# Kernel tuning notes

Hardware: AMD Instinct MI355X
Metric: run time of the kernel (lower is better)

Reference implementation:

```python
import jax, jax.numpy as jnp
import numpy as np

N, DIM = 512, 64
SIZE, QUANT = 3.0, 0.25
LXY = int((2 * SIZE + 1e-4) // QUANT)   # 24
LZ = int((2 * 2 + 1e-4) // QUANT)       # 16


def setup_inputs() -> dict:
    key = jax.random.key(0)
    ks = jax.random.split(key, 16)
    s = lambda d: 1.0 / np.sqrt(d)
    feat = jax.random.normal(ks[0], (N, DIM), jnp.float32)
    dxy = jax.random.uniform(ks[1], (N, N, 2), jnp.float32, -SIZE, SIZE)
    dz = jax.random.uniform(ks[2], (N, N, 1), jnp.float32, -2.0, 2.0)
    distance = jnp.concatenate([dxy, dz], axis=-1)
    return {
        "feat": feat,
        "distance": distance,
        "W_qkv": jax.random.normal(ks[3], (DIM, 3 * DIM), jnp.float32) * s(DIM),
        "b_qkv": jnp.zeros((3 * DIM,), jnp.float32),
        "Wg1": jax.random.normal(ks[4], (DIM, DIM), jnp.float32) * s(DIM),
        "bg1": jnp.zeros((DIM,), jnp.float32),
        "Wg2": jax.random.normal(ks[5], (DIM, DIM), jnp.float32) * s(DIM),
        "bg2": jnp.zeros((DIM,), jnp.float32),
        "table_x": jax.random.normal(ks[6], (3, LXY, DIM), jnp.float32) * 0.02,
        "table_y": jax.random.normal(ks[7], (3, LXY, DIM), jnp.float32) * 0.02,
        "table_z": jax.random.normal(ks[8], (3, LZ, DIM), jnp.float32) * 0.02,
        "Wd": jax.random.normal(ks[9], (3 * DIM, DIM), jnp.float32) * s(3 * DIM),
        "bd": jnp.zeros((DIM,), jnp.float32),
        "ln_g": jnp.ones((DIM,), jnp.float32),
        "ln_b": jnp.zeros((DIM,), jnp.float32),
    }


def _quant_idx(distance):
    ixy = jnp.minimum((distance[:, :, :2] + SIZE) // QUANT, 2.0 * SIZE / QUANT - 1)
    iz = jnp.minimum((distance[:, :, 2:] + 2.0) // QUANT, 4.0 / QUANT - 1)
    return jnp.concatenate([ixy, iz], axis=-1).astype(jnp.int32)  # [N,N,3]


def _vec_att(feat, idx, W_qkv, b_qkv, Wg1, bg1, Wg2, bg2, table_x, table_y, table_z):
    n, dim = feat.shape
    qkv = (feat @ W_qkv + b_qkv).reshape(n, 3, dim)
    q, k, v = qkv[:, 0], qkv[:, 1], qkv[:, 2]
    # relation MLP on pairwise q-k differences: [N,N,dim]
    rel = q[:, None, :] - k[None, :, :]
    rel = jnp.maximum(rel @ Wg1 + bg1, 0.0) @ Wg2 + bg2
    ix, iy, iz = idx[:, :, 0], idx[:, :, 1], idx[:, :, 2]
    enc_q = table_x[0][ix] + table_y[0][iy] + table_z[0][iz]
    enc_k = table_x[1][ix] + table_y[1][iy] + table_z[1][iz]
    enc_v = table_x[2][ix] + table_y[2][iy] + table_z[2][iz]
    rel = rel + q[:, None, :] * enc_q + k[None, :, :] * enc_k
    vv = v[None, :, :] + enc_v
    weights = jax.nn.softmax(rel, axis=1)
    return jnp.sum(weights * vv, axis=1)  # [N,dim]


def reference(feat, distance, W_qkv, b_qkv, Wg1, bg1, Wg2, bg2,
              table_x, table_y, table_z, Wd, bd, ln_g, ln_b):
    idx = _quant_idx(distance)
    att = _vec_att(feat, idx, W_qkv, b_qkv, Wg1, bg1, Wg2, bg2,
                   table_x, table_y, table_z)
    n = att.shape[0]
    mean_rep = jnp.broadcast_to(jnp.mean(att, axis=0, keepdims=True), att.shape)
    max_rep = jnp.broadcast_to(jnp.max(att, axis=0, keepdims=True), att.shape)
    x = jnp.concatenate([att, mean_rep, max_rep], axis=-1)  # [N, 3*dim]
    h = x @ Wd + bd
    mu = jnp.mean(h, axis=-1, keepdims=True)
    var = jnp.mean((h - mu) ** 2, axis=-1, keepdims=True)
    h = (h - mu) * jax.lax.rsqrt(var + 1e-5) * ln_g + ln_b
    return jnp.maximum(h, 0.0)
```

## Files before the change

kernel.cpp:

```cpp
#include <hip/hip_runtime.h>
#include <hip/hip_bf16.h>
#include <math.h>

#define N 512
#define DIM 64

typedef __attribute__((ext_vector_type(8))) short short8;
typedef __attribute__((ext_vector_type(4))) float f32x4;

#define WS_Q 0
#define WS_K (N*DIM)
#define WS_V (2*N*DIM)
#define WS_A (3*N*DIM)
#define WS_B (4*N*DIM)
#define WS_ATT (5*N*DIM)
#define WS_MEAN (6*N*DIM)
#define WS_MAXK (6*N*DIM + DIM)

__device__ __forceinline__ unsigned short f2bf(float f) {
    unsigned u = __float_as_uint(f);
    return (unsigned short)((u + 0x7fffu + ((u >> 16) & 1u)) >> 16);
}

__global__ void k_qkv(const float* __restrict__ feat, const float* __restrict__ Wqkv,
                      const float* __restrict__ bqkv, const float* __restrict__ Wg1,
                      const float* __restrict__ bg1, float* __restrict__ ws) {
    __shared__ float frow[DIM];
    __shared__ float qrow[DIM];
    __shared__ float krow[DIM];
    int i = blockIdx.x;
    int c = threadIdx.x;
    if (i == 0 && c < DIM) {
        ws[WS_MEAN + c] = 0.0f;
        ((unsigned*)ws)[WS_MAXK + c] = 0u;
    }
    if (c < DIM) frow[c] = feat[i * DIM + c];
    __syncthreads();
    float acc = bqkv[c];
#pragma unroll
    for (int kk = 0; kk < DIM; ++kk) acc += frow[kk] * Wqkv[kk * 3 * DIM + c];
    if (c < DIM) {
        ws[WS_Q + i * DIM + c] = acc;
        qrow[c] = acc;
    } else if (c < 2 * DIM) {
        ws[WS_K + i * DIM + (c - DIM)] = acc;
        krow[c - DIM] = acc;
    } else {
        ws[WS_V + i * DIM + (c - 2 * DIM)] = acc;
    }
    __syncthreads();
    if (c < DIM) {
        float a = bg1[c];
#pragma unroll
        for (int kk = 0; kk < DIM; ++kk) a += qrow[kk] * Wg1[kk * DIM + c];
        ws[WS_A + i * DIM + c] = a;
    } else if (c < 2 * DIM) {
        int cc = c - DIM;
        float b = 0.0f;
#pragma unroll
        for (int kk = 0; kk < DIM; ++kk) b += krow[kk] * Wg1[kk * DIM + cc];
        ws[WS_B + i * DIM + cc] = b;
    }
}

__global__ __launch_bounds__(256, 2) void k_attn(
    const float* __restrict__ dist,
    const float* __restrict__ tx, const float* __restrict__ ty,
    const float* __restrict__ tz, const float* __restrict__ Wg2,
    const float* __restrict__ bg2, float* __restrict__ ws) {
    __shared__ float stx[3 * 24 * 65];
    __shared__ float sty[3 * 24 * 65];
    __shared__ float stz[3 * 16 * 65];
    __shared__ int sidx[N];
    __shared__ float smrg[4][4][16][3];

    const int i = blockIdx.x;
    const int tid = threadIdx.x;
    const int w = tid >> 6;
    const int lane = tid & 63;
    const int l15 = lane & 15;
    const int kg = lane >> 4;

    for (int t = tid; t < 3 * 24 * 64; t += 256) {
        int row = t >> 6, col = t & 63;
        stx[row * 65 + col] = tx[t];
        sty[row * 65 + col] = ty[t];
    }
    for (int t = tid; t < 3 * 16 * 64; t += 256) {
        int row = t >> 6, col = t & 63;
        stz[row * 65 + col] = tz[t];
    }
    for (int j = tid; j < N; j += 256) {
        const float* dp = dist + ((size_t)i * N + j) * 3;
        int ix = min((int)floorf((dp[0] + 3.0f) * 4.0f), 23);
        int iy = min((int)floorf((dp[1] + 3.0f) * 4.0f), 23);
        int iz = min((int)floorf((dp[2] + 2.0f) * 4.0f), 15);
        sidx[j] = ix | (iy << 5) | (iz << 10);
    }

    short8 wB[2][4];
#pragma unroll
    for (int ks = 0; ks < 2; ++ks)
#pragma unroll
        for (int n = 0; n < 4; ++n) {
            union { short8 v; unsigned short u[8]; } tmp;
#pragma unroll
            for (int e = 0; e < 8; ++e)
                tmp.u[e] = f2bf(Wg2[(ks * 32 + kg * 8 + e) * DIM + n * 16 + l15]);
            wB[ks][n] = tmp.v;
        }

    float af[16];
    {
        const float* ap = ws + WS_A + i * DIM + kg * 8;
#pragma unroll
        for (int e = 0; e < 8; ++e) { af[e] = ap[e]; af[8 + e] = ap[32 + e]; }
    }
    float qr[4], br[4];
#pragma unroll
    for (int n = 0; n < 4; ++n) {
        qr[n] = ws[WS_Q + i * DIM + n * 16 + l15];
        br[n] = bg2[n * 16 + l15];
    }

    const float* Bp = ws + WS_B;
    const float* Kp = ws + WS_K;
    const float* Vp = ws + WS_V;

    float stm[4], stl[4], sta[4];
#pragma unroll
    for (int n = 0; n < 4; ++n) { stm[n] = -INFINITY; stl[n] = 0.f; sta[n] = 0.f; }

    __syncthreads();

    const float LOG2E = 1.4426950408889634f;

    for (int cb = 0; cb < N; cb += 64) {
        int jA = cb + w * 16 + l15;
        const float* bb = Bp + jA * DIM + kg * 8;
        union { short8 v; unsigned short u[8]; } h0, h1;
#pragma unroll
        for (int e = 0; e < 8; ++e) {
            h0.u[e] = f2bf(fmaxf(af[e] - bb[e], 0.f));
            h1.u[e] = f2bf(fmaxf(af[8 + e] - bb[32 + e], 0.f));
        }
        f32x4 acc[4];
#pragma unroll
        for (int n = 0; n < 4; ++n) {
            acc[n] = (f32x4)(0.f);
            acc[n] = __builtin_amdgcn_mfma_f32_16x16x32_bf16(h0.v, wB[0][n], acc[n], 0, 0, 0);
            acc[n] = __builtin_amdgcn_mfma_f32_16x16x32_bf16(h1.v, wB[1][n], acc[n], 0, 0, 0);
        }
        int j0 = cb + w * 16 + kg * 4;
        int pk[4];
#pragma unroll
        for (int r = 0; r < 4; ++r) pk[r] = sidx[j0 + r];
#pragma unroll
        for (int n = 0; n < 4; ++n) {
            int dof = n * 16 + l15;
            float rel2[4], vvv[4];
#pragma unroll
            for (int r = 0; r < 4; ++r) {
                int ix = pk[r] & 31, iy = (pk[r] >> 5) & 31, iz = pk[r] >> 10;
                float eq = stx[ix * 65 + dof] + sty[iy * 65 + dof] + stz[iz * 65 + dof];
                float ek = stx[(24 + ix) * 65 + dof] + sty[(24 + iy) * 65 + dof] +
                           stz[(16 + iz) * 65 + dof];
                float ev = stx[(48 + ix) * 65 + dof] + sty[(48 + iy) * 65 + dof] +
                           stz[(32 + iz) * 65 + dof];
                int j = j0 + r;
                float kv = Kp[j * DIM + dof];
                float vv = Vp[j * DIM + dof];
                float rel = acc[n][r] + br[n] + qr[n] * eq + kv * ek;
                rel2[r] = rel * LOG2E;
                vvv[r] = vv + ev;
            }
            float mx = fmaxf(fmaxf(rel2[0], rel2[1]), fmaxf(rel2[2], rel2[3]));
            float mn = fmaxf(stm[n], mx);
            float sc = exp2f(stm[n] - mn);
            float sl = 0.f, sa = 0.f;
#pragma unroll
            for (int r = 0; r < 4; ++r) {
                float p = exp2f(rel2[r] - mn);
                sl += p;
                sa += p * vvv[r];
            }
            stl[n] = stl[n] * sc + sl;
            sta[n] = sta[n] * sc + sa;
            stm[n] = mn;
        }
    }

#pragma unroll
    for (int n = 0; n < 4; ++n) {
#pragma unroll
        for (int off = 16; off <= 32; off <<= 1) {
            float om = __shfl_xor(stm[n], off);
            float ol = __shfl_xor(stl[n], off);
            float oa = __shfl_xor(sta[n], off);
            float mn = fmaxf(stm[n], om);
            float s1 = exp2f(stm[n] - mn), s2 = exp2f(om - mn);
            stl[n] = stl[n] * s1 + ol * s2;
            sta[n] = sta[n] * s1 + oa * s2;
            stm[n] = mn;
        }
        if (lane < 16) {
            smrg[w][n][l15][0] = stm[n];
            smrg[w][n][l15][1] = stl[n];
            smrg[w][n][l15][2] = sta[n];
        }
    }
    __syncthreads();
    if (tid < DIM) {
        int n = tid >> 4, c = tid & 15;
        float m = smrg[0][n][c][0], l = smrg[0][n][c][1], a = smrg[0][n][c][2];
#pragma unroll
        for (int ww = 1; ww < 4; ++ww) {
            float om = smrg[ww][n][c][0], ol = smrg[ww][n][c][1], oa = smrg[ww][n][c][2];
            float mn = fmaxf(m, om);
            float s1 = exp2f(m - mn), s2 = exp2f(om - mn);
            l = l * s1 + ol * s2;
            a = a * s1 + oa * s2;
            m = mn;
        }
        float att = a / l;
        ws[WS_ATT + i * DIM + tid] = att;
        atomicAdd(ws + WS_MEAN + tid, att);
        unsigned u = __float_as_uint(att);
        unsigned key = (u & 0x80000000u) ? ~u : (u | 0x80000000u);
        atomicMax((unsigned*)ws + WS_MAXK + tid, key);
    }
}

__global__ void k_final(const float* __restrict__ ws, const float* __restrict__ Wd,
                        const float* __restrict__ bd, const float* __restrict__ lng,
                        const float* __restrict__ lnb, float* __restrict__ out) {
    __shared__ float xs[3 * DIM];
    int i = blockIdx.x;
    int c = threadIdx.x;
    xs[c] = ws[WS_ATT + i * DIM + c];
    xs[DIM + c] = ws[WS_MEAN + c] * (1.0f / (float)N);
    unsigned key = ((const unsigned*)ws)[WS_MAXK + c];
    unsigned ub = (key & 0x80000000u) ? (key & 0x7fffffffu) : ~key;
    xs[2 * DIM + c] = __uint_as_float(ub);
    __syncthreads();
    float h = bd[c];
#pragma unroll
    for (int kk = 0; kk < 3 * DIM; ++kk) h += xs[kk] * Wd[kk * DIM + c];
    float s = h;
#pragma unroll
    for (int off = 32; off >= 1; off >>= 1) s += __shfl_xor(s, off);
    float mu = s * (1.0f / DIM);
    float dif = h - mu;
    float s2 = dif * dif;
#pragma unroll
    for (int off = 32; off >= 1; off >>= 1) s2 += __shfl_xor(s2, off);
    float var = s2 * (1.0f / DIM);
    float rs = rsqrtf(var + 1e-5f);
    float o = dif * rs * lng[c] + lnb[c];
    out[i * DIM + c] = fmaxf(o, 0.0f);
}

extern "C" void kernel_launch(void* const* d_in, const int* in_sizes, int n_in,
                              void* d_out, int out_size, void* d_ws, size_t ws_size,
                              hipStream_t stream) {
    (void)in_sizes; (void)n_in; (void)out_size; (void)ws_size;
    const float* feat = (const float*)d_in[0];
    const float* dist = (const float*)d_in[1];
    const float* Wqkv = (const float*)d_in[2];
    const float* bqkv = (const float*)d_in[3];
    const float* Wg1  = (const float*)d_in[4];
    const float* bg1  = (const float*)d_in[5];
    const float* Wg2  = (const float*)d_in[6];
    const float* bg2  = (const float*)d_in[7];
    const float* tx   = (const float*)d_in[8];
    const float* ty   = (const float*)d_in[9];
    const float* tz   = (const float*)d_in[10];
    const float* Wd   = (const float*)d_in[11];
    const float* bd   = (const float*)d_in[12];
    const float* lng  = (const float*)d_in[13];
    const float* lnb  = (const float*)d_in[14];
    float* ws = (float*)d_ws;
    float* out = (float*)d_out;

    hipLaunchKernelGGL(k_qkv, dim3(N), dim3(192), 0, stream, feat, Wqkv, bqkv, Wg1, bg1, ws);
    hipLaunchKernelGGL(k_attn, dim3(N), dim3(256), 0, stream, dist, tx, ty, tz, Wg2, bg2, ws);
    hipLaunchKernelGGL(k_final, dim3(N), dim3(64), 0, stream, ws, Wd, bd, lng, lnb, out);
}
```

Measured before the change: 141.5 us.

## Pack q/k tables as bf16 pairs, fold log2e, widen attention and final blocks

```diff
diff --git a/kernel.cpp b/kernel.cpp
--- a/kernel.cpp
+++ b/kernel.cpp
@@ -36,9 +36,15 @@
     }
     if (c < DIM) frow[c] = feat[i * DIM + c];
     __syncthreads();
-    float acc = bqkv[c];
-#pragma unroll
-    for (int kk = 0; kk < DIM; ++kk) acc += frow[kk] * Wqkv[kk * 3 * DIM + c];
+    float a0 = bqkv[c], a1 = 0.f, a2 = 0.f, a3 = 0.f;
+#pragma unroll
+    for (int kk = 0; kk < DIM; kk += 4) {
+        a0 += frow[kk + 0] * Wqkv[(kk + 0) * 3 * DIM + c];
+        a1 += frow[kk + 1] * Wqkv[(kk + 1) * 3 * DIM + c];
+        a2 += frow[kk + 2] * Wqkv[(kk + 2) * 3 * DIM + c];
+        a3 += frow[kk + 3] * Wqkv[(kk + 3) * 3 * DIM + c];
+    }
+    float acc = (a0 + a1) + (a2 + a3);
     if (c < DIM) {
         ws[WS_Q + i * DIM + c] = acc;
         qrow[c] = acc;
@@ -49,30 +55,36 @@
         ws[WS_V + i * DIM + (c - 2 * DIM)] = acc;
     }
     __syncthreads();
-    if (c < DIM) {
-        float a = bg1[c];
-#pragma unroll
-        for (int kk = 0; kk < DIM; ++kk) a += qrow[kk] * Wg1[kk * DIM + c];
-        ws[WS_A + i * DIM + c] = a;
-    } else if (c < 2 * DIM) {
-        int cc = c - DIM;
-        float b = 0.0f;
-#pragma unroll
-        for (int kk = 0; kk < DIM; ++kk) b += krow[kk] * Wg1[kk * DIM + cc];
-        ws[WS_B + i * DIM + cc] = b;
-    }
-}
-
-__global__ __launch_bounds__(256, 2) void k_attn(
+    if (c < 2 * DIM) {
+        const float* src = (c < DIM) ? qrow : krow;
+        int cc = (c < DIM) ? c : c - DIM;
+        float b0 = (c < DIM) ? bg1[c] : 0.0f, b1 = 0.f, b2 = 0.f, b3 = 0.f;
+#pragma unroll
+        for (int kk = 0; kk < DIM; kk += 4) {
+            b0 += src[kk + 0] * Wg1[(kk + 0) * DIM + cc];
+            b1 += src[kk + 1] * Wg1[(kk + 1) * DIM + cc];
+            b2 += src[kk + 2] * Wg1[(kk + 2) * DIM + cc];
+            b3 += src[kk + 3] * Wg1[(kk + 3) * DIM + cc];
+        }
+        float r = (b0 + b1) + (b2 + b3);
+        if (c < DIM) ws[WS_A + i * DIM + c] = r;
+        else         ws[WS_B + i * DIM + cc] = r;
+    }
+}
+
+__global__ __launch_bounds__(512, 4) void k_attn(
     const float* __restrict__ dist,
     const float* __restrict__ tx, const float* __restrict__ ty,
     const float* __restrict__ tz, const float* __restrict__ Wg2,
     const float* __restrict__ bg2, float* __restrict__ ws) {
-    __shared__ float stx[3 * 24 * 65];
-    __shared__ float sty[3 * 24 * 65];
-    __shared__ float stz[3 * 16 * 65];
+    __shared__ unsigned sxqk[24 * 65];
+    __shared__ unsigned syqk[24 * 65];
+    __shared__ unsigned szqk[16 * 65];
+    __shared__ float sxv[24 * 65];
+    __shared__ float syv[24 * 65];
+    __shared__ float szv[16 * 65];
     __shared__ int sidx[N];
-    __shared__ float smrg[4][4][16][3];
+    __shared__ float smrg[8][4][16][3];
 
     const int i = blockIdx.x;
     const int tid = threadIdx.x;
@@ -80,17 +92,24 @@
     const int lane = tid & 63;
     const int l15 = lane & 15;
     const int kg = lane >> 4;
-
-    for (int t = tid; t < 3 * 24 * 64; t += 256) {
-        int row = t >> 6, col = t & 63;
-        stx[row * 65 + col] = tx[t];
-        sty[row * 65 + col] = ty[t];
-    }
-    for (int t = tid; t < 3 * 16 * 64; t += 256) {
-        int row = t >> 6, col = t & 63;
-        stz[row * 65 + col] = tz[t];
-    }
-    for (int j = tid; j < N; j += 256) {
+    const float LOG2E = 1.4426950408889634f;
+
+    for (int t = tid; t < 24 * 64; t += 512) {
+        int row = t >> 6, d = t & 63, o = row * 65 + d;
+        sxqk[o] = (__float_as_uint(tx[t]) & 0xffff0000u) |
+                  (__float_as_uint(tx[1536 + t] * LOG2E) >> 16);
+        syqk[o] = (__float_as_uint(ty[t]) & 0xffff0000u) |
+                  (__float_as_uint(ty[1536 + t] * LOG2E) >> 16);
+        sxv[o] = tx[3072 + t];
+        syv[o] = ty[3072 + t];
+    }
+    for (int t = tid; t < 16 * 64; t += 512) {
+        int row = t >> 6, d = t & 63, o = row * 65 + d;
+        szqk[o] = (__float_as_uint(tz[t]) & 0xffff0000u) |
+                  (__float_as_uint(tz[1024 + t] * LOG2E) >> 16);
+        szv[o] = tz[2048 + t];
+    }
+    for (int j = tid; j < N; j += 512) {
         const float* dp = dist + ((size_t)i * N + j) * 3;
         int ix = min((int)floorf((dp[0] + 3.0f) * 4.0f), 23);
         int iy = min((int)floorf((dp[1] + 3.0f) * 4.0f), 23);
@@ -98,29 +117,30 @@
         sidx[j] = ix | (iy << 5) | (iz << 10);
     }
 
-    short8 wB[2][4];
-#pragma unroll
-    for (int ks = 0; ks < 2; ++ks)
-#pragma unroll
-        for (int n = 0; n < 4; ++n) {
+    short8 wB[4][2];
+#pragma unroll
+    for (int n = 0; n < 4; ++n)
+#pragma unroll
+        for (int ks = 0; ks < 2; ++ks) {
             union { short8 v; unsigned short u[8]; } tmp;
 #pragma unroll
             for (int e = 0; e < 8; ++e)
-                tmp.u[e] = f2bf(Wg2[(ks * 32 + kg * 8 + e) * DIM + n * 16 + l15]);
-            wB[ks][n] = tmp.v;
-        }
-
-    float af[16];
+                tmp.u[e] = f2bf(Wg2[(ks * 32 + kg * 8 + e) * DIM + n * 16 + l15] * LOG2E);
+            wB[n][ks] = tmp.v;
+        }
+    float af[2][8];
     {
         const float* ap = ws + WS_A + i * DIM + kg * 8;
 #pragma unroll
-        for (int e = 0; e < 8; ++e) { af[e] = ap[e]; af[8 + e] = ap[32 + e]; }
+        for (int ks = 0; ks < 2; ++ks)
+#pragma unroll
+            for (int e = 0; e < 8; ++e) af[ks][e] = ap[ks * 32 + e];
     }
     float qr[4], br[4];
 #pragma unroll
     for (int n = 0; n < 4; ++n) {
-        qr[n] = ws[WS_Q + i * DIM + n * 16 + l15];
-        br[n] = bg2[n * 16 + l15];
+        qr[n] = ws[WS_Q + i * DIM + n * 16 + l15] * LOG2E;
+        br[n] = bg2[n * 16 + l15] * LOG2E;
     }
 
     const float* Bp = ws + WS_B;
@@ -130,62 +150,68 @@
     float stm[4], stl[4], sta[4];
 #pragma unroll
     for (int n = 0; n < 4; ++n) { stm[n] = -INFINITY; stl[n] = 0.f; sta[n] = 0.f; }
-
-    __syncthreads();
-
-    const float LOG2E = 1.4426950408889634f;
-
-    for (int cb = 0; cb < N; cb += 64) {
-        int jA = cb + w * 16 + l15;
-        const float* bb = Bp + jA * DIM + kg * 8;
-        union { short8 v; unsigned short u[8]; } h0, h1;
-#pragma unroll
-        for (int e = 0; e < 8; ++e) {
-            h0.u[e] = f2bf(fmaxf(af[e] - bb[e], 0.f));
-            h1.u[e] = f2bf(fmaxf(af[8 + e] - bb[32 + e], 0.f));
+    __syncthreads();
+
+#pragma unroll
+    for (int t4 = 0; t4 < 4; ++t4) {
+        const int j0w = (w + 8 * t4) * 16;
+        short8 h[2];
+        {
+            const float* bb = Bp + (j0w + l15) * DIM + kg * 8;
+#pragma unroll
+            for (int ks = 0; ks < 2; ++ks) {
+                union { short8 v; unsigned short u[8]; } hh;
+#pragma unroll
+                for (int e = 0; e < 8; ++e)
+                    hh.u[e] = f2bf(fmaxf(af[ks][e] - bb[ks * 32 + e], 0.f));
+                h[ks] = hh.v;
+            }
         }
         f32x4 acc[4];
 #pragma unroll
         for (int n = 0; n < 4; ++n) {
-            acc[n] = (f32x4)(0.f);
-            acc[n] = __builtin_amdgcn_mfma_f32_16x16x32_bf16(h0.v, wB[0][n], acc[n], 0, 0, 0);
-            acc[n] = __builtin_amdgcn_mfma_f32_16x16x32_bf16(h1.v, wB[1][n], acc[n], 0, 0, 0);
-        }
-        int j0 = cb + w * 16 + kg * 4;
+            acc[n] = (f32x4)(br[n]);
+            acc[n] = __builtin_amdgcn_mfma_f32_16x16x32_bf16(h[0], wB[n][0], acc[n], 0, 0, 0);
+            acc[n] = __builtin_amdgcn_mfma_f32_16x16x32_bf16(h[1], wB[n][1], acc[n], 0, 0, 0);
+        }
         int pk[4];
 #pragma unroll
-        for (int r = 0; r < 4; ++r) pk[r] = sidx[j0 + r];
+        for (int rr = 0; rr < 4; ++rr) pk[rr] = sidx[j0w + kg * 4 + rr];
 #pragma unroll
         for (int n = 0; n < 4; ++n) {
-            int dof = n * 16 + l15;
+            const int dof = n * 16 + l15;
             float rel2[4], vvv[4];
 #pragma unroll
-            for (int r = 0; r < 4; ++r) {
-                int ix = pk[r] & 31, iy = (pk[r] >> 5) & 31, iz = pk[r] >> 10;
-                float eq = stx[ix * 65 + dof] + sty[iy * 65 + dof] + stz[iz * 65 + dof];
-                float ek = stx[(24 + ix) * 65 + dof] + sty[(24 + iy) * 65 + dof] +
-                           stz[(16 + iz) * 65 + dof];
-                float ev = stx[(48 + ix) * 65 + dof] + sty[(48 + iy) * 65 + dof] +
-                           stz[(32 + iz) * 65 + dof];
-                int j = j0 + r;
+            for (int rr = 0; rr < 4; ++rr) {
+                int ix = pk[rr] & 31, iy = (pk[rr] >> 5) & 31, iz = pk[rr] >> 10;
+                unsigned ux = sxqk[ix * 65 + dof];
+                unsigned uy = syqk[iy * 65 + dof];
+                unsigned uz = szqk[iz * 65 + dof];
+                float eq = __uint_as_float(ux & 0xffff0000u) +
+                           __uint_as_float(uy & 0xffff0000u) +
+                           __uint_as_float(uz & 0xffff0000u);
+                float ek = __uint_as_float(ux << 16) +
+                           __uint_as_float(uy << 16) +
+                           __uint_as_float(uz << 16);
+                float ev = sxv[ix * 65 + dof] + syv[iy * 65 + dof] + szv[iz * 65 + dof];
+                int j = j0w + kg * 4 + rr;
                 float kv = Kp[j * DIM + dof];
                 float vv = Vp[j * DIM + dof];
-                float rel = acc[n][r] + br[n] + qr[n] * eq + kv * ek;
-                rel2[r] = rel * LOG2E;
-                vvv[r] = vv + ev;
+                rel2[rr] = acc[n][rr] + qr[n] * eq + kv * ek;
+                vvv[rr] = vv + ev;
             }
             float mx = fmaxf(fmaxf(rel2[0], rel2[1]), fmaxf(rel2[2], rel2[3]));
             float mn = fmaxf(stm[n], mx);
             float sc = exp2f(stm[n] - mn);
             float sl = 0.f, sa = 0.f;
 #pragma unroll
-            for (int r = 0; r < 4; ++r) {
-                float p = exp2f(rel2[r] - mn);
+            for (int rr = 0; rr < 4; ++rr) {
+                float p = exp2f(rel2[rr] - mn);
                 sl += p;
-                sa += p * vvv[r];
+                sa = fmaf(p, vvv[rr], sa);
             }
-            stl[n] = stl[n] * sc + sl;
-            sta[n] = sta[n] * sc + sa;
+            stl[n] = fmaf(stl[n], sc, sl);
+            sta[n] = fmaf(sta[n], sc, sa);
             stm[n] = mn;
         }
     }
@@ -214,7 +240,7 @@
         int n = tid >> 4, c = tid & 15;
         float m = smrg[0][n][c][0], l = smrg[0][n][c][1], a = smrg[0][n][c][2];
 #pragma unroll
-        for (int ww = 1; ww < 4; ++ww) {
+        for (int ww = 1; ww < 8; ++ww) {
             float om = smrg[ww][n][c][0], ol = smrg[ww][n][c][1], oa = smrg[ww][n][c][2];
             float mn = fmaxf(m, om);
             float s1 = exp2f(m - mn), s2 = exp2f(om - mn);
@@ -235,29 +261,41 @@
                         const float* __restrict__ bd, const float* __restrict__ lng,
                         const float* __restrict__ lnb, float* __restrict__ out) {
     __shared__ float xs[3 * DIM];
+    __shared__ float hp[4][DIM];
     int i = blockIdx.x;
-    int c = threadIdx.x;
-    xs[c] = ws[WS_ATT + i * DIM + c];
-    xs[DIM + c] = ws[WS_MEAN + c] * (1.0f / (float)N);
-    unsigned key = ((const unsigned*)ws)[WS_MAXK + c];
-    unsigned ub = (key & 0x80000000u) ? (key & 0x7fffffffu) : ~key;
-    xs[2 * DIM + c] = __uint_as_float(ub);
-    __syncthreads();
-    float h = bd[c];
-#pragma unroll
-    for (int kk = 0; kk < 3 * DIM; ++kk) h += xs[kk] * Wd[kk * DIM + c];
-    float s = h;
-#pragma unroll
-    for (int off = 32; off >= 1; off >>= 1) s += __shfl_xor(s, off);
-    float mu = s * (1.0f / DIM);
-    float dif = h - mu;
-    float s2 = dif * dif;
-#pragma unroll
-    for (int off = 32; off >= 1; off >>= 1) s2 += __shfl_xor(s2, off);
-    float var = s2 * (1.0f / DIM);
-    float rs = rsqrtf(var + 1e-5f);
-    float o = dif * rs * lng[c] + lnb[c];
-    out[i * DIM + c] = fmaxf(o, 0.0f);
+    int tid = threadIdx.x;
+    int c = tid & 63, q = tid >> 6;
+    if (tid < DIM) xs[tid] = ws[WS_ATT + i * DIM + tid];
+    else if (tid < 2 * DIM) xs[tid] = ws[WS_MEAN + (tid - DIM)] * (1.0f / (float)N);
+    else if (tid < 3 * DIM) {
+        unsigned key = ((const unsigned*)ws)[WS_MAXK + (tid - 2 * DIM)];
+        unsigned ub = (key & 0x80000000u) ? (key & 0x7fffffffu) : ~key;
+        xs[tid] = __uint_as_float(ub);
+    }
+    __syncthreads();
+    float p0 = (q == 0) ? bd[c] : 0.0f, p1 = 0.f;
+#pragma unroll
+    for (int kk = q * 48; kk < q * 48 + 48; kk += 2) {
+        p0 += xs[kk] * Wd[kk * DIM + c];
+        p1 += xs[kk + 1] * Wd[(kk + 1) * DIM + c];
+    }
+    hp[q][c] = p0 + p1;
+    __syncthreads();
+    if (tid < DIM) {
+        float h = hp[0][tid] + hp[1][tid] + hp[2][tid] + hp[3][tid];
+        float s = h;
+#pragma unroll
+        for (int off = 32; off >= 1; off >>= 1) s += __shfl_xor(s, off);
+        float mu = s * (1.0f / DIM);
+        float dif = h - mu;
+        float s2 = dif * dif;
+#pragma unroll
+        for (int off = 32; off >= 1; off >>= 1) s2 += __shfl_xor(s2, off);
+        float var = s2 * (1.0f / DIM);
+        float rs = rsqrtf(var + 1e-5f);
+        float o = dif * rs * lng[tid] + lnb[tid];
+        out[i * DIM + tid] = fmaxf(o, 0.0f);
+    }
 }
 
 extern "C" void kernel_launch(void* const* d_in, const int* in_sizes, int n_in,
@@ -283,6 +321,6 @@
     float* out = (float*)d_out;
 
     hipLaunchKernelGGL(k_qkv, dim3(N), dim3(192), 0, stream, feat, Wqkv, bqkv, Wg1, bg1, ws);
-    hipLaunchKernelGGL(k_attn, dim3(N), dim3(256), 0, stream, dist, tx, ty, tz, Wg2, bg2, ws);
-    hipLaunchKernelGGL(k_final, dim3(N), dim3(64), 0, stream, ws, Wd, bd, lng, lnb, out);
-}
+    hipLaunchKernelGGL(k_attn, dim3(N), dim3(512), 0, stream, dist, tx, ty, tz, Wg2, bg2, ws);
+    hipLaunchKernelGGL(k_final, dim3(N), dim3(256), 0, stream, ws, Wd, bd, lng, lnb, out);
+}
```

Measured after the change: 450.1 us. 218% more time.
